# Performance work log

Measured on AMD Instinct MI355X. Metric: run time of the kernel, lower is better.

Reference implementation:

```python
import jax, jax.numpy as jnp
import numpy as np

CHUNK = 64  # rows of A processed per step; bounds the [CHUNK,K,N] intermediate


def setup_inputs() -> dict:
    key = jax.random.key(0)
    k1, k2, k3 = jax.random.split(key, 3)
    in_features, out_features = 768, 768
    x = jax.random.normal(k1, (2, 1024, in_features), dtype=jnp.float32)
    # kaiming_uniform_(a=sqrt(5)) on [out,in] -> bound = 1/sqrt(in_features)
    wb = 1.0 / np.sqrt(in_features)
    weight = jax.random.uniform(k2, (out_features, in_features), minval=-wb, maxval=wb, dtype=jnp.float32)
    bias = jax.random.uniform(k3, (out_features,), minval=-wb, maxval=wb, dtype=jnp.float32)
    return {"x": x, "weight": weight, "bias": bias}


def _mam(A, B):
    # A: [M, K], B: [K, N]. C[i,j] = max_k A[i,k]*B[k,j] + min_k A[i,k]*B[k,j]
    M, K = A.shape
    N = B.shape[1]
    def chunk_fn(a):  # a: [CHUNK, K]
        p = a[:, :, None] * B[None, :, :]  # [CHUNK, K, N]
        return jnp.max(p, axis=1) + jnp.min(p, axis=1)
    n_chunks = M // CHUNK
    C = jax.lax.map(chunk_fn, A.reshape(n_chunks, CHUNK, K))  # [n_chunks, CHUNK, N]
    return C.reshape(M, N)


def reference(x, weight, bias):
    # beta = 0 path: pure MAM + bias (matches MAMDense.forward with beta=False)
    K = x.shape[-1]
    x_flat = x.reshape(-1, K)               # [M, K]
    C = _mam(x_flat, weight.T)              # [M, N]
    C = C + bias[None, :]
    return C.reshape(x.shape[:-1] + (weight.shape[0],))
```

## Files before the change

### kernel.cpp

```cpp
#include <hip/hip_runtime.h>
#include <math.h>


#define M_DIM 2048
#define N_DIM 768
#define K_DIM 768

#define BM 64
#define BN 32
#define BK 64
#define KP (BK / 2)
#define NTILES (K_DIM / BK)

#define SAH 68
#define SBH 34

typedef _Float16 h2 __attribute__((ext_vector_type(2)));
typedef _Float16 h4 __attribute__((ext_vector_type(4)));
typedef _Float16 h8 __attribute__((ext_vector_type(8)));

__device__ __forceinline__ h2 cvt_pk(float x, float y) {
    return __builtin_bit_cast(h2, __builtin_amdgcn_cvt_pkrtz(x, y));
}

__global__ __launch_bounds__(256, 3) void mam_kernel(
    const float* __restrict__ A, const float* __restrict__ W,
    const float* __restrict__ bias, float* __restrict__ out)
{
    __shared__ __align__(16) h2 As[2][KP * SAH];
    __shared__ __align__(16) h2 Bs[2][KP * SBH];

    const int tid = threadIdx.x;
    const int m0 = blockIdx.y * BM;
    const int n0 = blockIdx.x * BN;
    const int mt = tid >> 4;
    const int nt = tid & 15;

    h2 pmax[4][2], pmin[4][2];
    const _Float16 HMIN = (_Float16)(-65504.0f), HMAX = (_Float16)(65504.0f);
#pragma unroll
    for (int i = 0; i < 4; ++i)
#pragma unroll
        for (int j = 0; j < 2; ++j) {
            pmax[i][j] = (h2){HMIN, HMIN};
            pmin[i][j] = (h2){HMAX, HMAX};
        }

    const int arow = tid >> 4;
    const int akc  = tid & 15;
    const float* Ap = A + (size_t)(m0 + arow) * K_DIM + akc * 4;
    const float* Wp = W + (size_t)(n0 + arow) * K_DIM + akc * 4;

    const float bb0 = bias[n0 + nt * 2 + 0];
    const float bb1 = bias[n0 + nt * 2 + 1];

    float4 pa0, pa1, pa2, pa3, pb0, pb1;

#define GLOAD(t) do {                                                        \
        const float* An_ = Ap + (t) * BK;                                    \
        const float* Wn_ = Wp + (t) * BK;                                    \
        pa0 = *(const float4*)(An_ + (size_t)( 0) * K_DIM);                  \
        pa1 = *(const float4*)(An_ + (size_t)(16) * K_DIM);                  \
        pa2 = *(const float4*)(An_ + (size_t)(32) * K_DIM);                  \
        pa3 = *(const float4*)(An_ + (size_t)(48) * K_DIM);                  \
        pb0 = *(const float4*)(Wn_ + (size_t)( 0) * K_DIM);                  \
        pb1 = *(const float4*)(Wn_ + (size_t)(16) * K_DIM);                  \
    } while (0)

#define SWRITE(buf) do {                                                     \
        h2* Aw_ = &As[buf][2 * akc * SAH + arow];                            \
        Aw_[0]            = cvt_pk(pa0.x, pa0.y);                            \
        Aw_[SAH]          = cvt_pk(pa0.z, pa0.w);                            \
        Aw_[16]           = cvt_pk(pa1.x, pa1.y);                            \
        Aw_[SAH + 16]     = cvt_pk(pa1.z, pa1.w);                            \
        Aw_[32]           = cvt_pk(pa2.x, pa2.y);                            \
        Aw_[SAH + 32]     = cvt_pk(pa2.z, pa2.w);                            \
        Aw_[48]           = cvt_pk(pa3.x, pa3.y);                            \
        Aw_[SAH + 48]     = cvt_pk(pa3.z, pa3.w);                            \
        h2* Bw_ = &Bs[buf][2 * akc * SBH + arow];                            \
        Bw_[0]            = cvt_pk(pb0.x, pb0.y);                            \
        Bw_[SBH]          = cvt_pk(pb0.z, pb0.w);                            \
        Bw_[16]           = cvt_pk(pb1.x, pb1.y);                            \
        Bw_[SBH + 16]     = cvt_pk(pb1.z, pb1.w);                            \
    } while (0)

#define COMPUTE(buf) do {                                                    \
        const h2* Ab_ = &As[buf][mt * 4];                                    \
        const h2* Bb_ = &Bs[buf][nt * 2];                                    \
        _Pragma("unroll")                                                    \
        for (int kk2 = 0; kk2 < KP; ++kk2) {                                 \
            const h8 a_ = *(const h8*)(Ab_ + kk2 * SAH);                     \
            const h4 b_ = *(const h4*)(Bb_ + kk2 * SBH);                     \
            const h2 am0 = __builtin_shufflevector(a_, a_, 0, 1);            \
            const h2 am1 = __builtin_shufflevector(a_, a_, 2, 3);            \
            const h2 am2 = __builtin_shufflevector(a_, a_, 4, 5);            \
            const h2 am3 = __builtin_shufflevector(a_, a_, 6, 7);            \
            const h2 bn0 = __builtin_shufflevector(b_, b_, 0, 1);            \
            const h2 bn1 = __builtin_shufflevector(b_, b_, 2, 3);            \
            h2 p_;                                                           \
            p_ = am0 * bn0; pmax[0][0] = __builtin_elementwise_max(pmax[0][0], p_); pmin[0][0] = __builtin_elementwise_min(pmin[0][0], p_); \
            p_ = am0 * bn1; pmax[0][1] = __builtin_elementwise_max(pmax[0][1], p_); pmin[0][1] = __builtin_elementwise_min(pmin[0][1], p_); \
            p_ = am1 * bn0; pmax[1][0] = __builtin_elementwise_max(pmax[1][0], p_); pmin[1][0] = __builtin_elementwise_min(pmin[1][0], p_); \
            p_ = am1 * bn1; pmax[1][1] = __builtin_elementwise_max(pmax[1][1], p_); pmin[1][1] = __builtin_elementwise_min(pmin[1][1], p_); \
            p_ = am2 * bn0; pmax[2][0] = __builtin_elementwise_max(pmax[2][0], p_); pmin[2][0] = __builtin_elementwise_min(pmin[2][0], p_); \
            p_ = am2 * bn1; pmax[2][1] = __builtin_elementwise_max(pmax[2][1], p_); pmin[2][1] = __builtin_elementwise_min(pmin[2][1], p_); \
            p_ = am3 * bn0; pmax[3][0] = __builtin_elementwise_max(pmax[3][0], p_); pmin[3][0] = __builtin_elementwise_min(pmin[3][0], p_); \
            p_ = am3 * bn1; pmax[3][1] = __builtin_elementwise_max(pmax[3][1], p_); pmin[3][1] = __builtin_elementwise_min(pmin[3][1], p_); \
        }                                                                    \
    } while (0)

    GLOAD(0);
    SWRITE(0);
    __syncthreads();

#pragma unroll 1
    for (int ktt = 0; ktt < NTILES / 2 - 1; ++ktt) {
        GLOAD(2 * ktt + 1);
        COMPUTE(0);
        SWRITE(1);
        __syncthreads();
        GLOAD(2 * ktt + 2);
        COMPUTE(1);
        SWRITE(0);
        __syncthreads();
    }
    GLOAD(NTILES - 1);
    COMPUTE(0);
    SWRITE(1);
    __syncthreads();
    COMPUTE(1);

#pragma unroll
    for (int i = 0; i < 4; ++i) {
        float2 o;
        o.x = fmaxf((float)pmax[i][0].x, (float)pmax[i][0].y)
            + fminf((float)pmin[i][0].x, (float)pmin[i][0].y) + bb0;
        o.y = fmaxf((float)pmax[i][1].x, (float)pmax[i][1].y)
            + fminf((float)pmin[i][1].x, (float)pmin[i][1].y) + bb1;
        *(float2*)&out[(size_t)(m0 + mt * 4 + i) * N_DIM + n0 + nt * 2] = o;
    }
}

extern "C" void kernel_launch(void* const* d_in, const int* in_sizes, int n_in,
                              void* d_out, int out_size, void* d_ws, size_t ws_size,
                              hipStream_t stream) {
    const float* x    = (const float*)d_in[0];
    const float* w    = (const float*)d_in[1];
    const float* bias = (const float*)d_in[2];
    float* out = (float*)d_out;

    dim3 grid(N_DIM / BN, M_DIM / BM);
    mam_kernel<<<grid, 256, 0, stream>>>(x, w, bias, out);
}
```

Measured before the change: 69.29 us.

## Split K across four thread groups with 4x4 register tiles and LDS reduction

Each 64x32 tile is now computed by 512 threads split into four groups, and each group handles a quarter of every K tile with a 4x4 (packed half2) register micro-tile instead of 4x2. Partial max/min results are merged through shared memory in a two-level tree, and group 0 writes float4 outputs. XOR swizzling of the LDS layout is added to reduce bank conflicts on the wider reads. The aim is to raise arithmetic intensity per LDS read and increase the number of resident waves. The cost is extra synchronisation and LDS traffic in the epilogue, plus higher register use under the 512-thread launch bound.

```diff
diff --git a/kernel.cpp b/kernel.cpp
--- a/kernel.cpp
+++ b/kernel.cpp
@@ -9,104 +9,114 @@
 #define BM 64
 #define BN 32
 #define BK 64
-#define KP (BK / 2)
-#define NTILES (K_DIM / BK)
+#define KP 32
+#define NTILES 12
 
 #define SAH 68
-#define SBH 34
+#define SBH 36
+#define ASZ (KP * SAH)
+#define BSZ (KP * SBH)
+#define EPI_STRIDE 36
+#define EPI_REGION (128 * EPI_STRIDE)
 
 typedef _Float16 h2 __attribute__((ext_vector_type(2)));
-typedef _Float16 h4 __attribute__((ext_vector_type(4)));
 typedef _Float16 h8 __attribute__((ext_vector_type(8)));
 
 __device__ __forceinline__ h2 cvt_pk(float x, float y) {
     return __builtin_bit_cast(h2, __builtin_amdgcn_cvt_pkrtz(x, y));
 }
-
-__global__ __launch_bounds__(256, 3) void mam_kernel(
+__device__ __forceinline__ h2 h2max(h2 a, h2 b) { return __builtin_elementwise_max(a, b); }
+__device__ __forceinline__ h2 h2min(h2 a, h2 b) { return __builtin_elementwise_min(a, b); }
+
+__global__ __launch_bounds__(512, 6) void mam_kernel(
     const float* __restrict__ A, const float* __restrict__ W,
     const float* __restrict__ bias, float* __restrict__ out)
 {
-    __shared__ __align__(16) h2 As[2][KP * SAH];
-    __shared__ __align__(16) h2 Bs[2][KP * SBH];
+    __shared__ __align__(16) unsigned char smem[36864];
+    h2* Ash = (h2*)smem;
+    h2* Bsh = (h2*)(smem + 2 * ASZ * 4);
+    float* epi = (float*)smem;
 
     const int tid = threadIdx.x;
+    const int g   = tid >> 7;
+    const int lid = tid & 127;
+    const int mt  = lid >> 3;
+    const int nt  = lid & 7;
     const int m0 = blockIdx.y * BM;
     const int n0 = blockIdx.x * BN;
-    const int mt = tid >> 4;
-    const int nt = tid & 15;
-
-    h2 pmax[4][2], pmin[4][2];
+
+    h2 pmax[4][4], pmin[4][4];
     const _Float16 HMIN = (_Float16)(-65504.0f), HMAX = (_Float16)(65504.0f);
 #pragma unroll
     for (int i = 0; i < 4; ++i)
 #pragma unroll
-        for (int j = 0; j < 2; ++j) {
+        for (int j = 0; j < 4; ++j) {
             pmax[i][j] = (h2){HMIN, HMIN};
             pmin[i][j] = (h2){HMAX, HMAX};
         }
 
     const int arow = tid >> 4;
     const int akc  = tid & 15;
+    const int aswz = 4 * (akc & 7);
+    const int awr  = arow ^ aswz;
     const float* Ap = A + (size_t)(m0 + arow) * K_DIM + akc * 4;
     const float* Wp = W + (size_t)(n0 + arow) * K_DIM + akc * 4;
 
-    const float bb0 = bias[n0 + nt * 2 + 0];
-    const float bb1 = bias[n0 + nt * 2 + 1];
-
-    float4 pa0, pa1, pa2, pa3, pb0, pb1;
-
-#define GLOAD(t) do {                                                        \
-        const float* An_ = Ap + (t) * BK;                                    \
-        const float* Wn_ = Wp + (t) * BK;                                    \
-        pa0 = *(const float4*)(An_ + (size_t)( 0) * K_DIM);                  \
-        pa1 = *(const float4*)(An_ + (size_t)(16) * K_DIM);                  \
-        pa2 = *(const float4*)(An_ + (size_t)(32) * K_DIM);                  \
-        pa3 = *(const float4*)(An_ + (size_t)(48) * K_DIM);                  \
-        pb0 = *(const float4*)(Wn_ + (size_t)( 0) * K_DIM);                  \
-        pb1 = *(const float4*)(Wn_ + (size_t)(16) * K_DIM);                  \
-    } while (0)
-
-#define SWRITE(buf) do {                                                     \
-        h2* Aw_ = &As[buf][2 * akc * SAH + arow];                            \
-        Aw_[0]            = cvt_pk(pa0.x, pa0.y);                            \
-        Aw_[SAH]          = cvt_pk(pa0.z, pa0.w);                            \
-        Aw_[16]           = cvt_pk(pa1.x, pa1.y);                            \
-        Aw_[SAH + 16]     = cvt_pk(pa1.z, pa1.w);                            \
-        Aw_[32]           = cvt_pk(pa2.x, pa2.y);                            \
-        Aw_[SAH + 32]     = cvt_pk(pa2.z, pa2.w);                            \
-        Aw_[48]           = cvt_pk(pa3.x, pa3.y);                            \
-        Aw_[SAH + 48]     = cvt_pk(pa3.z, pa3.w);                            \
-        h2* Bw_ = &Bs[buf][2 * akc * SBH + arow];                            \
-        Bw_[0]            = cvt_pk(pb0.x, pb0.y);                            \
-        Bw_[SBH]          = cvt_pk(pb0.z, pb0.w);                            \
-        Bw_[16]           = cvt_pk(pb1.x, pb1.y);                            \
-        Bw_[SBH + 16]     = cvt_pk(pb1.z, pb1.w);                            \
-    } while (0)
-
-#define COMPUTE(buf) do {                                                    \
-        const h2* Ab_ = &As[buf][mt * 4];                                    \
-        const h2* Bb_ = &Bs[buf][nt * 2];                                    \
-        _Pragma("unroll")                                                    \
-        for (int kk2 = 0; kk2 < KP; ++kk2) {                                 \
-            const h8 a_ = *(const h8*)(Ab_ + kk2 * SAH);                     \
-            const h4 b_ = *(const h4*)(Bb_ + kk2 * SBH);                     \
-            const h2 am0 = __builtin_shufflevector(a_, a_, 0, 1);            \
-            const h2 am1 = __builtin_shufflevector(a_, a_, 2, 3);            \
-            const h2 am2 = __builtin_shufflevector(a_, a_, 4, 5);            \
-            const h2 am3 = __builtin_shufflevector(a_, a_, 6, 7);            \
-            const h2 bn0 = __builtin_shufflevector(b_, b_, 0, 1);            \
-            const h2 bn1 = __builtin_shufflevector(b_, b_, 2, 3);            \
-            h2 p_;                                                           \
-            p_ = am0 * bn0; pmax[0][0] = __builtin_elementwise_max(pmax[0][0], p_); pmin[0][0] = __builtin_elementwise_min(pmin[0][0], p_); \
-            p_ = am0 * bn1; pmax[0][1] = __builtin_elementwise_max(pmax[0][1], p_); pmin[0][1] = __builtin_elementwise_min(pmin[0][1], p_); \
-            p_ = am1 * bn0; pmax[1][0] = __builtin_elementwise_max(pmax[1][0], p_); pmin[1][0] = __builtin_elementwise_min(pmin[1][0], p_); \
-            p_ = am1 * bn1; pmax[1][1] = __builtin_elementwise_max(pmax[1][1], p_); pmin[1][1] = __builtin_elementwise_min(pmin[1][1], p_); \
-            p_ = am2 * bn0; pmax[2][0] = __builtin_elementwise_max(pmax[2][0], p_); pmin[2][0] = __builtin_elementwise_min(pmin[2][0], p_); \
-            p_ = am2 * bn1; pmax[2][1] = __builtin_elementwise_max(pmax[2][1], p_); pmin[2][1] = __builtin_elementwise_min(pmin[2][1], p_); \
-            p_ = am3 * bn0; pmax[3][0] = __builtin_elementwise_max(pmax[3][0], p_); pmin[3][0] = __builtin_elementwise_min(pmin[3][0], p_); \
-            p_ = am3 * bn1; pmax[3][1] = __builtin_elementwise_max(pmax[3][1], p_); pmin[3][1] = __builtin_elementwise_min(pmin[3][1], p_); \
-        }                                                                    \
+    const float4 bv = *(const float4*)(bias + n0 + nt * 4);
+
+    unsigned aoff[4], boff[4];
+#pragma unroll
+    for (int u = 0; u < 4; ++u) {
+        const int c = 4 * (((g << 2) + u) & 7);
+        aoff[u] = (unsigned)((g * 8 + 2 * u) * SAH + ((4 * mt) ^ c));
+        boff[u] = (unsigned)((g * 8 + 2 * u) * SBH + ((4 * nt) ^ c));
+    }
+
+    float4 pa0, pa1, pb0;
+
+#define GLOAD(t) do {                                                         \
+        const float* An_ = Ap + (t) * BK;                                     \
+        pa0 = *(const float4*)(An_);                                          \
+        pa1 = *(const float4*)(An_ + (size_t)32 * K_DIM);                     \
+        pb0 = *(const float4*)(Wp + (t) * BK);                                \
+    } while (0)
+
+#define SWRITE(buf) do {                                                      \
+        h2* Aw_ = Ash + (buf) * ASZ + 2 * akc * SAH + awr;                    \
+        Aw_[0]        = cvt_pk(pa0.x, pa0.y);                                 \
+        Aw_[SAH]      = cvt_pk(pa0.z, pa0.w);                                 \
+        Aw_[32]       = cvt_pk(pa1.x, pa1.y);                                 \
+        Aw_[SAH + 32] = cvt_pk(pa1.z, pa1.w);                                 \
+        h2* Bw_ = Bsh + (buf) * BSZ + 2 * akc * SBH + awr;                    \
+        Bw_[0]        = cvt_pk(pb0.x, pb0.y);                                 \
+        Bw_[SBH]      = cvt_pk(pb0.z, pb0.w);                                 \
+    } while (0)
+
+#define COMPUTE(buf) do {                                                     \
+        _Pragma("unroll")                                                     \
+        for (int s = 0; s < 8; ++s) {                                         \
+            const int u_ = s >> 1, o_ = s & 1;                                \
+            const h8 a_ = *(const h8*)(Ash + (buf) * ASZ + aoff[u_] + o_ * SAH); \
+            const h8 b_ = *(const h8*)(Bsh + (buf) * BSZ + boff[u_] + o_ * SBH); \
+            const h2 am[4] = {__builtin_shufflevector(a_, a_, 0, 1),          \
+                              __builtin_shufflevector(a_, a_, 2, 3),          \
+                              __builtin_shufflevector(a_, a_, 4, 5),          \
+                              __builtin_shufflevector(a_, a_, 6, 7)};         \
+            const h2 bn[4] = {__builtin_shufflevector(b_, b_, 0, 1),          \
+                              __builtin_shufflevector(b_, b_, 2, 3),          \
+                              __builtin_shufflevector(b_, b_, 4, 5),          \
+                              __builtin_shufflevector(b_, b_, 6, 7)};         \
+            _Pragma("unroll")                                                 \
+            for (int i_ = 0; i_ < 4; ++i_)                                    \
+            {                                                                 \
+                _Pragma("unroll")                                             \
+                for (int j_ = 0; j_ < 4; ++j_) {                              \
+                    const h2 p_ = am[i_] * bn[j_];                            \
+                    pmax[i_][j_] = h2max(pmax[i_][j_], p_);                   \
+                    pmin[i_][j_] = h2min(pmin[i_][j_], p_);                   \
+                }                                                             \
+            }                                                                 \
+        }                                                                     \
     } while (0)
 
     GLOAD(0);
@@ -130,14 +140,63 @@
     __syncthreads();
     COMPUTE(1);
 
-#pragma unroll
-    for (int i = 0; i < 4; ++i) {
-        float2 o;
-        o.x = fmaxf((float)pmax[i][0].x, (float)pmax[i][0].y)
-            + fminf((float)pmin[i][0].x, (float)pmin[i][0].y) + bb0;
-        o.y = fmaxf((float)pmax[i][1].x, (float)pmax[i][1].y)
-            + fminf((float)pmin[i][1].x, (float)pmin[i][1].y) + bb1;
-        *(float2*)&out[(size_t)(m0 + mt * 4 + i) * N_DIM + n0 + nt * 2] = o;
+#define EPI_PACK(dst) do {                                                    \
+        float* w_ = (dst);                                                    \
+        _Pragma("unroll")                                                     \
+        for (int i_ = 0; i_ < 4; ++i_) {                                      \
+            float4 vx_, vn_;                                                  \
+            vx_.x = __builtin_bit_cast(float, pmax[i_][0]);                   \
+            vx_.y = __builtin_bit_cast(float, pmax[i_][1]);                   \
+            vx_.z = __builtin_bit_cast(float, pmax[i_][2]);                   \
+            vx_.w = __builtin_bit_cast(float, pmax[i_][3]);                   \
+            vn_.x = __builtin_bit_cast(float, pmin[i_][0]);                   \
+            vn_.y = __builtin_bit_cast(float, pmin[i_][1]);                   \
+            vn_.z = __builtin_bit_cast(float, pmin[i_][2]);                   \
+            vn_.w = __builtin_bit_cast(float, pmin[i_][3]);                   \
+            *(float4*)(w_ + i_ * 4)      = vx_;                               \
+            *(float4*)(w_ + 16 + i_ * 4) = vn_;                               \
+        }                                                                     \
+    } while (0)
+
+#define EPI_COMBINE(src) do {                                                 \
+        const float* r_ = (src);                                              \
+        _Pragma("unroll")                                                     \
+        for (int i_ = 0; i_ < 4; ++i_) {                                      \
+            const float4 vx_ = *(const float4*)(r_ + i_ * 4);                 \
+            const float4 vn_ = *(const float4*)(r_ + 16 + i_ * 4);            \
+            pmax[i_][0] = h2max(pmax[i_][0], __builtin_bit_cast(h2, vx_.x));  \
+            pmax[i_][1] = h2max(pmax[i_][1], __builtin_bit_cast(h2, vx_.y));  \
+            pmax[i_][2] = h2max(pmax[i_][2], __builtin_bit_cast(h2, vx_.z));  \
+            pmax[i_][3] = h2max(pmax[i_][3], __builtin_bit_cast(h2, vx_.w));  \
+            pmin[i_][0] = h2min(pmin[i_][0], __builtin_bit_cast(h2, vn_.x));  \
+            pmin[i_][1] = h2min(pmin[i_][1], __builtin_bit_cast(h2, vn_.y));  \
+            pmin[i_][2] = h2min(pmin[i_][2], __builtin_bit_cast(h2, vn_.z));  \
+            pmin[i_][3] = h2min(pmin[i_][3], __builtin_bit_cast(h2, vn_.w));  \
+        }                                                                     \
+    } while (0)
+
+    __syncthreads();
+    if (g >= 2) EPI_PACK(epi + (size_t)(g - 2) * EPI_REGION + lid * EPI_STRIDE);
+    __syncthreads();
+    if (g < 2)  EPI_COMBINE(epi + (size_t)g * EPI_REGION + lid * EPI_STRIDE);
+    __syncthreads();
+    if (g == 1) EPI_PACK(epi + lid * EPI_STRIDE);
+    __syncthreads();
+    if (g == 0) {
+        EPI_COMBINE(epi + lid * EPI_STRIDE);
+#pragma unroll
+        for (int i = 0; i < 4; ++i) {
+            float4 o;
+            o.x = fmaxf((float)pmax[i][0].x, (float)pmax[i][0].y)
+                + fminf((float)pmin[i][0].x, (float)pmin[i][0].y) + bv.x;
+            o.y = fmaxf((float)pmax[i][1].x, (float)pmax[i][1].y)
+                + fminf((float)pmin[i][1].x, (float)pmin[i][1].y) + bv.y;
+            o.z = fmaxf((float)pmax[i][2].x, (float)pmax[i][2].y)
+                + fminf((float)pmin[i][2].x, (float)pmin[i][2].y) + bv.z;
+            o.w = fmaxf((float)pmax[i][3].x, (float)pmax[i][3].y)
+                + fminf((float)pmin[i][3].x, (float)pmin[i][3].y) + bv.w;
+            *(float4*)&out[(size_t)(m0 + mt * 4 + i) * N_DIM + n0 + nt * 4] = o;
+        }
     }
 }
 
@@ -150,5 +209,5 @@
     float* out = (float*)d_out;
 
     dim3 grid(N_DIM / BN, M_DIM / BM);
-    mam_kernel<<<grid, 256, 0, stream>>>(x, w, bias, out);
+    mam_kernel<<<grid, 512, 0, stream>>>(x, w, bias, out);
 }
```

Measured after the change: 87.56 us. +26.4%, slower.

## Split K four ways with fp16 max/min workspace combine, larger 64x64 tiles, swizzled LDS

Applied to the files above, without the earlier changes.

Widens each block's tile to 64x64 with a 4x4 per-thread register tile, so each LDS operand load feeds more packed-half products. It adds an XOR swizzle on LDS columns and drops double buffering in favour of a single buffer with two barriers per tile. With enough workspace, K is split four ways across grid z. Each split writes its packed half max and min to workspace, and a second kernel reduces the four partials and adds bias. The intent is to restore occupancy and parallelism lost by the larger tile, at the cost of an extra launch and workspace traffic.

```diff
diff --git a/kernel.cpp b/kernel.cpp
--- a/kernel.cpp
+++ b/kernel.cpp
@@ -5,140 +5,206 @@
 #define M_DIM 2048
 #define N_DIM 768
 #define K_DIM 768
+#define NOUT (M_DIM * N_DIM)
 
 #define BM 64
-#define BN 32
+#define BN 64
 #define BK 64
-#define KP (BK / 2)
-#define NTILES (K_DIM / BK)
-
+#define KP 32
 #define SAH 68
-#define SBH 34
+#define SBH 68
 
 typedef _Float16 h2 __attribute__((ext_vector_type(2)));
-typedef _Float16 h4 __attribute__((ext_vector_type(4)));
 typedef _Float16 h8 __attribute__((ext_vector_type(8)));
 
 __device__ __forceinline__ h2 cvt_pk(float x, float y) {
     return __builtin_bit_cast(h2, __builtin_amdgcn_cvt_pkrtz(x, y));
 }
-
-__global__ __launch_bounds__(256, 3) void mam_kernel(
+__device__ __forceinline__ h2 h2max(h2 a, h2 b) { return __builtin_elementwise_max(a, b); }
+__device__ __forceinline__ h2 h2min(h2 a, h2 b) { return __builtin_elementwise_min(a, b); }
+__device__ __forceinline__ unsigned packmm(h2 px, h2 pn) {
+    h2 r;
+    r.x = px.x >= px.y ? px.x : px.y;
+    r.y = pn.x <= pn.y ? pn.x : pn.y;
+    return __builtin_bit_cast(unsigned, r);
+}
+
+template <int NSPL>
+__global__ __launch_bounds__(256, 6) void mam_main(
     const float* __restrict__ A, const float* __restrict__ W,
-    const float* __restrict__ bias, float* __restrict__ out)
+    const float* __restrict__ bias, float* __restrict__ out,
+    unsigned* __restrict__ ws)
 {
-    __shared__ __align__(16) h2 As[2][KP * SAH];
-    __shared__ __align__(16) h2 Bs[2][KP * SBH];
+    __shared__ __align__(16) h2 As[KP * SAH];
+    __shared__ __align__(16) h2 Bs[KP * SBH];
 
     const int tid = threadIdx.x;
-    const int m0 = blockIdx.y * BM;
-    const int n0 = blockIdx.x * BN;
-    const int mt = tid >> 4;
-    const int nt = tid & 15;
-
-    h2 pmax[4][2], pmin[4][2];
+    const int m0  = blockIdx.y * BM;
+    const int n0  = blockIdx.x * BN;
+    const int NT  = 12 / NSPL;
+    const int kb  = blockIdx.z * NT * BK;
+
+    const int mt  = tid >> 4;
+    const int nt  = tid & 15;
+    const int am4 = 4 * mt;
+    const int bn4 = 4 * nt;
+
+    h2 pmax[4][4], pmin[4][4];
     const _Float16 HMIN = (_Float16)(-65504.0f), HMAX = (_Float16)(65504.0f);
 #pragma unroll
     for (int i = 0; i < 4; ++i)
 #pragma unroll
-        for (int j = 0; j < 2; ++j) {
+        for (int j = 0; j < 4; ++j) {
             pmax[i][j] = (h2){HMIN, HMIN};
             pmin[i][j] = (h2){HMAX, HMAX};
         }
 
     const int arow = tid >> 4;
     const int akc  = tid & 15;
-    const float* Ap = A + (size_t)(m0 + arow) * K_DIM + akc * 4;
-    const float* Wp = W + (size_t)(n0 + arow) * K_DIM + akc * 4;
-
-    const float bb0 = bias[n0 + nt * 2 + 0];
-    const float bb1 = bias[n0 + nt * 2 + 1];
-
-    float4 pa0, pa1, pa2, pa3, pb0, pb1;
+    const int swz  = 4 * (akc & 7);
+    const float* Ap = A + (size_t)(m0 + arow) * K_DIM + kb + akc * 4;
+    const float* Wp = W + (size_t)(n0 + arow) * K_DIM + kb + akc * 4;
+
+    float4 pa0, pa1, pa2, pa3, pb0, pb1, pb2, pb3;
 
 #define GLOAD(t) do {                                                        \
         const float* An_ = Ap + (t) * BK;                                    \
         const float* Wn_ = Wp + (t) * BK;                                    \
-        pa0 = *(const float4*)(An_ + (size_t)( 0) * K_DIM);                  \
-        pa1 = *(const float4*)(An_ + (size_t)(16) * K_DIM);                  \
-        pa2 = *(const float4*)(An_ + (size_t)(32) * K_DIM);                  \
-        pa3 = *(const float4*)(An_ + (size_t)(48) * K_DIM);                  \
-        pb0 = *(const float4*)(Wn_ + (size_t)( 0) * K_DIM);                  \
-        pb1 = *(const float4*)(Wn_ + (size_t)(16) * K_DIM);                  \
-    } while (0)
-
-#define SWRITE(buf) do {                                                     \
-        h2* Aw_ = &As[buf][2 * akc * SAH + arow];                            \
-        Aw_[0]            = cvt_pk(pa0.x, pa0.y);                            \
-        Aw_[SAH]          = cvt_pk(pa0.z, pa0.w);                            \
-        Aw_[16]           = cvt_pk(pa1.x, pa1.y);                            \
-        Aw_[SAH + 16]     = cvt_pk(pa1.z, pa1.w);                            \
-        Aw_[32]           = cvt_pk(pa2.x, pa2.y);                            \
-        Aw_[SAH + 32]     = cvt_pk(pa2.z, pa2.w);                            \
-        Aw_[48]           = cvt_pk(pa3.x, pa3.y);                            \
-        Aw_[SAH + 48]     = cvt_pk(pa3.z, pa3.w);                            \
-        h2* Bw_ = &Bs[buf][2 * akc * SBH + arow];                            \
-        Bw_[0]            = cvt_pk(pb0.x, pb0.y);                            \
-        Bw_[SBH]          = cvt_pk(pb0.z, pb0.w);                            \
-        Bw_[16]           = cvt_pk(pb1.x, pb1.y);                            \
-        Bw_[SBH + 16]     = cvt_pk(pb1.z, pb1.w);                            \
-    } while (0)
-
-#define COMPUTE(buf) do {                                                    \
-        const h2* Ab_ = &As[buf][mt * 4];                                    \
-        const h2* Bb_ = &Bs[buf][nt * 2];                                    \
+        pa0 = *(const float4*)(An_ + (size_t) 0 * K_DIM);                    \
+        pa1 = *(const float4*)(An_ + (size_t)16 * K_DIM);                    \
+        pa2 = *(const float4*)(An_ + (size_t)32 * K_DIM);                    \
+        pa3 = *(const float4*)(An_ + (size_t)48 * K_DIM);                    \
+        pb0 = *(const float4*)(Wn_ + (size_t) 0 * K_DIM);                    \
+        pb1 = *(const float4*)(Wn_ + (size_t)16 * K_DIM);                    \
+        pb2 = *(const float4*)(Wn_ + (size_t)32 * K_DIM);                    \
+        pb3 = *(const float4*)(Wn_ + (size_t)48 * K_DIM);                    \
+    } while (0)
+
+#define SWRITE() do {                                                        \
+        h2* Aw_ = As + 2 * akc * SAH;                                        \
+        h2* Bw_ = Bs + 2 * akc * SBH;                                        \
+        const int c0_ = (arow +  0) ^ swz;                                   \
+        const int c1_ = (arow + 16) ^ swz;                                   \
+        const int c2_ = (arow + 32) ^ swz;                                   \
+        const int c3_ = (arow + 48) ^ swz;                                   \
+        Aw_[c0_]       = cvt_pk(pa0.x, pa0.y);                               \
+        Aw_[SAH + c0_] = cvt_pk(pa0.z, pa0.w);                               \
+        Aw_[c1_]       = cvt_pk(pa1.x, pa1.y);                               \
+        Aw_[SAH + c1_] = cvt_pk(pa1.z, pa1.w);                               \
+        Aw_[c2_]       = cvt_pk(pa2.x, pa2.y);                               \
+        Aw_[SAH + c2_] = cvt_pk(pa2.z, pa2.w);                               \
+        Aw_[c3_]       = cvt_pk(pa3.x, pa3.y);                               \
+        Aw_[SAH + c3_] = cvt_pk(pa3.z, pa3.w);                               \
+        Bw_[c0_]       = cvt_pk(pb0.x, pb0.y);                               \
+        Bw_[SBH + c0_] = cvt_pk(pb0.z, pb0.w);                               \
+        Bw_[c1_]       = cvt_pk(pb1.x, pb1.y);                               \
+        Bw_[SBH + c1_] = cvt_pk(pb1.z, pb1.w);                               \
+        Bw_[c2_]       = cvt_pk(pb2.x, pb2.y);                               \
+        Bw_[SBH + c2_] = cvt_pk(pb2.z, pb2.w);                               \
+        Bw_[c3_]       = cvt_pk(pb3.x, pb3.y);                               \
+        Bw_[SBH + c3_] = cvt_pk(pb3.z, pb3.w);                               \
+    } while (0)
+
+#define COMPUTE() do {                                                       \
         _Pragma("unroll")                                                    \
         for (int kk2 = 0; kk2 < KP; ++kk2) {                                 \
-            const h8 a_ = *(const h8*)(Ab_ + kk2 * SAH);                     \
-            const h4 b_ = *(const h4*)(Bb_ + kk2 * SBH);                     \
+            const int cc_ = 4 * ((kk2 >> 1) & 7);                            \
+            const h8 a_ = *(const h8*)(As + kk2 * SAH + (am4 ^ cc_));        \
+            const h8 b_ = *(const h8*)(Bs + kk2 * SBH + (bn4 ^ cc_));        \
             const h2 am0 = __builtin_shufflevector(a_, a_, 0, 1);            \
             const h2 am1 = __builtin_shufflevector(a_, a_, 2, 3);            \
             const h2 am2 = __builtin_shufflevector(a_, a_, 4, 5);            \
             const h2 am3 = __builtin_shufflevector(a_, a_, 6, 7);            \
             const h2 bn0 = __builtin_shufflevector(b_, b_, 0, 1);            \
             const h2 bn1 = __builtin_shufflevector(b_, b_, 2, 3);            \
+            const h2 bn2 = __builtin_shufflevector(b_, b_, 4, 5);            \
+            const h2 bn3 = __builtin_shufflevector(b_, b_, 6, 7);            \
             h2 p_;                                                           \
-            p_ = am0 * bn0; pmax[0][0] = __builtin_elementwise_max(pmax[0][0], p_); pmin[0][0] = __builtin_elementwise_min(pmin[0][0], p_); \
-            p_ = am0 * bn1; pmax[0][1] = __builtin_elementwise_max(pmax[0][1], p_); pmin[0][1] = __builtin_elementwise_min(pmin[0][1], p_); \
-            p_ = am1 * bn0; pmax[1][0] = __builtin_elementwise_max(pmax[1][0], p_); pmin[1][0] = __builtin_elementwise_min(pmin[1][0], p_); \
-            p_ = am1 * bn1; pmax[1][1] = __builtin_elementwise_max(pmax[1][1], p_); pmin[1][1] = __builtin_elementwise_min(pmin[1][1], p_); \
-            p_ = am2 * bn0; pmax[2][0] = __builtin_elementwise_max(pmax[2][0], p_); pmin[2][0] = __builtin_elementwise_min(pmin[2][0], p_); \
-            p_ = am2 * bn1; pmax[2][1] = __builtin_elementwise_max(pmax[2][1], p_); pmin[2][1] = __builtin_elementwise_min(pmin[2][1], p_); \
-            p_ = am3 * bn0; pmax[3][0] = __builtin_elementwise_max(pmax[3][0], p_); pmin[3][0] = __builtin_elementwise_min(pmin[3][0], p_); \
-            p_ = am3 * bn1; pmax[3][1] = __builtin_elementwise_max(pmax[3][1], p_); pmin[3][1] = __builtin_elementwise_min(pmin[3][1], p_); \
+            p_ = am0 * bn0; pmax[0][0] = h2max(pmax[0][0], p_); pmin[0][0] = h2min(pmin[0][0], p_); \
+            p_ = am0 * bn1; pmax[0][1] = h2max(pmax[0][1], p_); pmin[0][1] = h2min(pmin[0][1], p_); \
+            p_ = am0 * bn2; pmax[0][2] = h2max(pmax[0][2], p_); pmin[0][2] = h2min(pmin[0][2], p_); \
+            p_ = am0 * bn3; pmax[0][3] = h2max(pmax[0][3], p_); pmin[0][3] = h2min(pmin[0][3], p_); \
+            p_ = am1 * bn0; pmax[1][0] = h2max(pmax[1][0], p_); pmin[1][0] = h2min(pmin[1][0], p_); \
+            p_ = am1 * bn1; pmax[1][1] = h2max(pmax[1][1], p_); pmin[1][1] = h2min(pmin[1][1], p_); \
+            p_ = am1 * bn2; pmax[1][2] = h2max(pmax[1][2], p_); pmin[1][2] = h2min(pmin[1][2], p_); \
+            p_ = am1 * bn3; pmax[1][3] = h2max(pmax[1][3], p_); pmin[1][3] = h2min(pmin[1][3], p_); \
+            p_ = am2 * bn0; pmax[2][0] = h2max(pmax[2][0], p_); pmin[2][0] = h2min(pmin[2][0], p_); \
+            p_ = am2 * bn1; pmax[2][1] = h2max(pmax[2][1], p_); pmin[2][1] = h2min(pmin[2][1], p_); \
+            p_ = am2 * bn2; pmax[2][2] = h2max(pmax[2][2], p_); pmin[2][2] = h2min(pmin[2][2], p_); \
+            p_ = am2 * bn3; pmax[2][3] = h2max(pmax[2][3], p_); pmin[2][3] = h2min(pmin[2][3], p_); \
+            p_ = am3 * bn0; pmax[3][0] = h2max(pmax[3][0], p_); pmin[3][0] = h2min(pmin[3][0], p_); \
+            p_ = am3 * bn1; pmax[3][1] = h2max(pmax[3][1], p_); pmin[3][1] = h2min(pmin[3][1], p_); \
+            p_ = am3 * bn2; pmax[3][2] = h2max(pmax[3][2], p_); pmin[3][2] = h2min(pmin[3][2], p_); \
+            p_ = am3 * bn3; pmax[3][3] = h2max(pmax[3][3], p_); pmin[3][3] = h2min(pmin[3][3], p_); \
         }                                                                    \
     } while (0)
 
     GLOAD(0);
-    SWRITE(0);
+    SWRITE();
     __syncthreads();
-
 #pragma unroll 1
-    for (int ktt = 0; ktt < NTILES / 2 - 1; ++ktt) {
-        GLOAD(2 * ktt + 1);
-        COMPUTE(0);
-        SWRITE(1);
+    for (int t = 0; t < NT - 1; ++t) {
+        COMPUTE();
+        GLOAD(t + 1);
         __syncthreads();
-        GLOAD(2 * ktt + 2);
-        COMPUTE(1);
-        SWRITE(0);
+        SWRITE();
         __syncthreads();
     }
-    GLOAD(NTILES - 1);
-    COMPUTE(0);
-    SWRITE(1);
-    __syncthreads();
-    COMPUTE(1);
-
-#pragma unroll
-    for (int i = 0; i < 4; ++i) {
-        float2 o;
-        o.x = fmaxf((float)pmax[i][0].x, (float)pmax[i][0].y)
-            + fminf((float)pmin[i][0].x, (float)pmin[i][0].y) + bb0;
-        o.y = fmaxf((float)pmax[i][1].x, (float)pmax[i][1].y)
-            + fminf((float)pmin[i][1].x, (float)pmin[i][1].y) + bb1;
-        *(float2*)&out[(size_t)(m0 + mt * 4 + i) * N_DIM + n0 + nt * 2] = o;
+    COMPUTE();
+
+    if (NSPL == 1) {
+        const float4 bv = *(const float4*)(bias + n0 + bn4);
+#pragma unroll
+        for (int i = 0; i < 4; ++i) {
+            float4 o;
+            o.x = fmaxf((float)pmax[i][0].x, (float)pmax[i][0].y)
+                + fminf((float)pmin[i][0].x, (float)pmin[i][0].y) + bv.x;
+            o.y = fmaxf((float)pmax[i][1].x, (float)pmax[i][1].y)
+                + fminf((float)pmin[i][1].x, (float)pmin[i][1].y) + bv.y;
+            o.z = fmaxf((float)pmax[i][2].x, (float)pmax[i][2].y)
+                + fminf((float)pmin[i][2].x, (float)pmin[i][2].y) + bv.z;
+            o.w = fmaxf((float)pmax[i][3].x, (float)pmax[i][3].y)
+                + fminf((float)pmin[i][3].x, (float)pmin[i][3].y) + bv.w;
+            *(float4*)&out[(size_t)(m0 + am4 + i) * N_DIM + n0 + bn4] = o;
+        }
+    } else {
+        unsigned* wp = ws + (size_t)blockIdx.z * NOUT
+                          + (size_t)(m0 + am4) * N_DIM + n0 + bn4;
+#pragma unroll
+        for (int i = 0; i < 4; ++i) {
+            uint4 v;
+            v.x = packmm(pmax[i][0], pmin[i][0]);
+            v.y = packmm(pmax[i][1], pmin[i][1]);
+            v.z = packmm(pmax[i][2], pmin[i][2]);
+            v.w = packmm(pmax[i][3], pmin[i][3]);
+            *(uint4*)(wp + (size_t)i * N_DIM) = v;
+        }
     }
+}
+
+__global__ __launch_bounds__(256) void mam_combine(
+    const unsigned* __restrict__ ws, const float* __restrict__ bias,
+    float* __restrict__ out)
+{
+    const int i4 = (blockIdx.x * 256 + threadIdx.x) * 4;
+    const uint4 v0 = *(const uint4*)(ws + (size_t)0 * NOUT + i4);
+    const uint4 v1 = *(const uint4*)(ws + (size_t)1 * NOUT + i4);
+    const uint4 v2 = *(const uint4*)(ws + (size_t)2 * NOUT + i4);
+    const uint4 v3 = *(const uint4*)(ws + (size_t)3 * NOUT + i4);
+    const float4 bv = *(const float4*)(bias + (i4 % N_DIM));
+    float4 o;
+#define CMB(e) do {                                                          \
+        const h2 a_ = __builtin_bit_cast(h2, v0.e);                          \
+        const h2 b_ = __builtin_bit_cast(h2, v1.e);                          \
+        const h2 c_ = __builtin_bit_cast(h2, v2.e);                          \
+        const h2 d_ = __builtin_bit_cast(h2, v3.e);                          \
+        const h2 mx_ = h2max(h2max(a_, b_), h2max(c_, d_));                  \
+        const h2 mn_ = h2min(h2min(a_, b_), h2min(c_, d_));                  \
+        o.e = (float)mx_.x + (float)mn_.y + bv.e;                            \
+    } while (0)
+    CMB(x); CMB(y); CMB(z); CMB(w);
+#undef CMB
+    *(float4*)(out + i4) = o;
 }
 
 extern "C" void kernel_launch(void* const* d_in, const int* in_sizes, int n_in,
@@ -149,6 +215,14 @@
     const float* bias = (const float*)d_in[2];
     float* out = (float*)d_out;
 
-    dim3 grid(N_DIM / BN, M_DIM / BM);
-    mam_kernel<<<grid, 256, 0, stream>>>(x, w, bias, out);
-}
+    const size_t need = (size_t)4 * NOUT * sizeof(unsigned);
+    if (ws_size >= need) {
+        mam_main<4><<<dim3(N_DIM / BN, M_DIM / BM, 4), 256, 0, stream>>>(
+            x, w, bias, out, (unsigned*)d_ws);
+        mam_combine<<<NOUT / 4 / 256, 256, 0, stream>>>(
+            (const unsigned*)d_ws, bias, out);
+    } else {
+        mam_main<1><<<dim3(N_DIM / BN, M_DIM / BM, 1), 256, 0, stream>>>(
+            x, w, bias, out, nullptr);
+    }
+}
```

Result: slower. 75.25 us (+8.6%).
